# Optimization experiments

Measured on AMD Instinct MI355X. Metric: run time of the kernel, lower is better.

The kernel has to match this reference:

```python
import jax, jax.numpy as jnp
import numpy as np

N_NODES = 100000
N_EDGES = 800000
F_IN = 128
HID = 128
HEADS = 4
HEAD_DIM = HID // HEADS
LAYERS = 3
N_CLASSES = 40
NEG_SLOPE = 0.2
BN_EPS = 1e-5


def setup_inputs() -> dict:
    key = jax.random.key(0)
    ks = jax.random.split(key, 10)
    feat = jax.random.normal(ks[0], (N_NODES, F_IN), dtype=jnp.float32)
    src = jax.random.randint(ks[1], (N_EDGES,), 0, N_NODES, dtype=jnp.int32)
    dst = jax.random.randint(ks[2], (N_EDGES,), 0, N_NODES, dtype=jnp.int32)
    W_enc = jax.random.normal(ks[3], (F_IN, HID), dtype=jnp.float32) / np.sqrt(F_IN)
    b_enc = jnp.zeros((HID,), dtype=jnp.float32)
    Ws = jax.random.normal(ks[4], (LAYERS, HID, HID), dtype=jnp.float32) / np.sqrt(HID)
    attn_ls = jax.random.normal(ks[5], (LAYERS, HEADS, HEAD_DIM), dtype=jnp.float32) / np.sqrt(HEAD_DIM)
    attn_rs = jax.random.normal(ks[6], (LAYERS, HEADS, HEAD_DIM), dtype=jnp.float32) / np.sqrt(HEAD_DIM)
    biases = jnp.zeros((LAYERS, HID), dtype=jnp.float32)
    gammas = jnp.ones((LAYERS, HID), dtype=jnp.float32)
    betas = jnp.zeros((LAYERS, HID), dtype=jnp.float32)
    W_pred = jax.random.normal(ks[7], (HID, N_CLASSES), dtype=jnp.float32) / np.sqrt(HID)
    b_pred = jnp.zeros((N_CLASSES,), dtype=jnp.float32)
    return {"feat": feat, "src": src, "dst": dst, "W_enc": W_enc, "b_enc": b_enc,
            "Ws": Ws, "attn_ls": attn_ls, "attn_rs": attn_rs, "biases": biases,
            "gammas": gammas, "betas": betas, "W_pred": W_pred, "b_pred": b_pred}


def _gat_layer(h, src, dst, W, a_l, a_r, bias, n_nodes):
    # h: [N, HID] -> projected per-head features [N, H, D]
    hf = (h @ W).reshape(n_nodes, HEADS, HEAD_DIM)
    el = jnp.sum(hf * a_l, axis=-1)  # [N, H]
    er = jnp.sum(hf * a_r, axis=-1)  # [N, H]
    e = jax.nn.leaky_relu(el[src] + er[dst], NEG_SLOPE)  # [E, H]
    # edge softmax over incoming edges of each destination node
    m = jax.ops.segment_max(e, dst, num_segments=n_nodes)  # [N, H]
    ex = jnp.exp(e - m[dst])
    s = jax.ops.segment_sum(ex, dst, num_segments=n_nodes)  # [N, H]
    alpha = ex / s[dst]  # [E, H]
    msg = hf[src] * alpha[:, :, None]  # [E, H, D]
    out = jax.ops.segment_sum(msg, dst, num_segments=n_nodes)  # [N, H, D]
    return out.reshape(n_nodes, HEADS * HEAD_DIM) + bias


def _batchnorm(x, gamma, beta):
    mean = jnp.mean(x, axis=0)
    var = jnp.var(x, axis=0)
    return gamma * (x - mean) * jax.lax.rsqrt(var + BN_EPS) + beta


def reference(feat, src, dst, W_enc, b_enc, Ws, attn_ls, attn_rs, biases, gammas, betas, W_pred, b_pred):
    n_nodes = feat.shape[0]
    h = jax.nn.relu(feat @ W_enc + b_enc)
    h_last = None
    for i in range(Ws.shape[0]):
        h = _gat_layer(h, src, dst, Ws[i], attn_ls[i], attn_rs[i], biases[i], n_nodes)
        if h_last is not None:
            h = h + h_last
        h_last = h
        h = _batchnorm(h, gammas[i], betas[i])
        h = jax.nn.relu(h)
    return h @ W_pred + b_pred
```

## Files before the change

kernel.cpp:

```cpp
#include <hip/hip_runtime.h>

typedef __attribute__((ext_vector_type(8))) short short8;
typedef __attribute__((ext_vector_type(4))) float f32x4;

#define N_NODES 100000
#define N_EDGES 800000
#define NEG 0.2f
#define BN_EPS 1e-5f
#define AGG_GRID 2048

__device__ __forceinline__ ushort bf16b(float f) {
  unsigned u = __float_as_uint(f);
  return (ushort)((u + 0x7FFFu + ((u >> 16) & 1u)) >> 16);
}
__device__ __forceinline__ float bflo(unsigned u) { return __uint_as_float(u << 16); }
__device__ __forceinline__ float bfhi(unsigned u) { return __uint_as_float(u & 0xFFFF0000u); }

__global__ void k_hist(const int* __restrict__ dst, int* __restrict__ cnt, int e) {
  int i = blockIdx.x * blockDim.x + threadIdx.x;
  if (i < e) atomicAdd(&cnt[dst[i]], 1);
}

__global__ void k_scan1(const int* __restrict__ cnt, int* __restrict__ rowptr,
                        int* __restrict__ bsums, int n) {
  __shared__ int sm[256];
  int i = blockIdx.x * 256 + threadIdx.x;
  int v = (i < n) ? cnt[i] : 0;
  sm[threadIdx.x] = v;
  __syncthreads();
  for (int off = 1; off < 256; off <<= 1) {
    int t = (threadIdx.x >= off) ? sm[threadIdx.x - off] : 0;
    __syncthreads();
    sm[threadIdx.x] += t;
    __syncthreads();
  }
  if (i < n) rowptr[i + 1] = sm[threadIdx.x];
  if (threadIdx.x == 255) bsums[blockIdx.x] = sm[255];
}

__global__ void k_scan2(int* __restrict__ bsums, int nb) {
  __shared__ int sm[512];
  int v = (threadIdx.x < nb) ? bsums[threadIdx.x] : 0;
  sm[threadIdx.x] = v;
  __syncthreads();
  for (int off = 1; off < 512; off <<= 1) {
    int t = (threadIdx.x >= off) ? sm[threadIdx.x - off] : 0;
    __syncthreads();
    sm[threadIdx.x] += t;
    __syncthreads();
  }
  if (threadIdx.x < nb) bsums[threadIdx.x] = sm[threadIdx.x] - v;
}

__global__ void k_scan3(int* __restrict__ rowptr, const int* __restrict__ bsums,
                        int* __restrict__ cursor, int n) {
  int i = blockIdx.x * 256 + threadIdx.x;
  if (i < n) {
    int val = rowptr[i + 1] + bsums[blockIdx.x];
    rowptr[i + 1] = val;
    if (i + 1 < n) cursor[i + 1] = val;
  }
  if (i == 0) { rowptr[0] = 0; cursor[0] = 0; }
}

__global__ void k_scatter(const int* __restrict__ src, const int* __restrict__ dst,
                          int* __restrict__ cursor, int2* __restrict__ esort, int e) {
  int i = blockIdx.x * blockDim.x + threadIdx.x;
  if (i < e) {
    int d = dst[i];
    int pos = atomicAdd(&cursor[d], 1);
    esort[pos] = make_int2(src[i], d);
  }
}

__global__ void k_packW(const float* __restrict__ W_enc, const float* __restrict__ Ws,
                        ushort* __restrict__ Wp) {
  int s = blockIdx.x * 256 + threadIdx.x;
  int wi = s >> 11, s2 = s & 2047;
  int kt = s2 >> 9, nb8 = (s2 >> 6) & 7, l = s2 & 63;
  const float* Wsrc = (wi == 0) ? W_enc : Ws + (size_t)(wi - 1) * 16384;
  int n = nb8 * 16 + (l & 15);
  int k0 = kt * 32 + (l >> 4) * 8;
  unsigned pk[4];
#pragma unroll
  for (int j = 0; j < 4; ++j) {
    ushort lo = bf16b(Wsrc[(size_t)(k0 + 2 * j) * 128 + n]);
    ushort hi = bf16b(Wsrc[(size_t)(k0 + 2 * j + 1) * 128 + n]);
    pk[j] = (unsigned)lo | ((unsigned)hi << 16);
  }
  *(uint4*)&Wp[(size_t)s * 8] = make_uint4(pk[0], pk[1], pk[2], pk[3]);
}

template <int MODE>
__global__ __launch_bounds__(256) void k_mgemm(
    const float* __restrict__ Af, const ushort* __restrict__ Ab,
    const ushort* __restrict__ Wp, const float* __restrict__ bias,
    const float* __restrict__ stats, const float* __restrict__ al,
    const float* __restrict__ ar, float* __restrict__ el, float* __restrict__ er,
    ushort* __restrict__ Cb) {
  __shared__ __align__(16) ushort Al[32 * 128];
  int tid = threadIdx.x;
  int lane = tid & 63, w = tid >> 6;
  int wr = w & 1, wc = w >> 1;
  int l15 = lane & 15, l4 = lane >> 4;
  int rb = blockIdx.x * 32;

  const uint4* wp4 = (const uint4*)Wp;
  short8 bfr[4][4];
#pragma unroll
  for (int kt = 0; kt < 4; ++kt) {
#pragma unroll
    for (int nb = 0; nb < 4; ++nb) {
      uint4 t = wp4[(size_t)((kt * 8 + wc * 4 + nb) * 64 + lane)];
      bfr[kt][nb] = *(short8*)&t;
    }
  }

  {
    int row = tid >> 3;
    int c16 = (tid & 7) * 16;
    int kc0 = (tid & 7) * 2;
    char* base = (char*)Al + row * 256;
    if (MODE == 1) {
      const uint4* srcp = (const uint4*)(Ab + (size_t)(rb + row) * 128 + c16);
      uint4 v0 = srcp[0], v1 = srcp[1];
      *(uint4*)(base + ((kc0 ^ (row & 7)) << 4)) = v0;
      *(uint4*)(base + (((kc0 + 1) ^ (row & 7)) << 4)) = v1;
    } else if (MODE == 2) {
      const uint4* srcp = (const uint4*)(Ab + (size_t)(rb + row) * 128 + c16);
      uint4 v0 = srcp[0], v1 = srcp[1];
      unsigned pk[8];
#pragma unroll
      for (int j = 0; j < 4; ++j) {
        unsigned wv = ((const unsigned*)&v0)[j];
        float2 sc = *(const float2*)&stats[c16 + 2 * j];
        float2 sh = *(const float2*)&stats[128 + c16 + 2 * j];
        float x0 = fmaxf(bflo(wv) * sc.x + sh.x, 0.f);
        float x1 = fmaxf(bfhi(wv) * sc.y + sh.y, 0.f);
        pk[j] = (unsigned)bf16b(x0) | ((unsigned)bf16b(x1) << 16);
      }
#pragma unroll
      for (int j = 0; j < 4; ++j) {
        unsigned wv = ((const unsigned*)&v1)[j];
        float2 sc = *(const float2*)&stats[c16 + 8 + 2 * j];
        float2 sh = *(const float2*)&stats[128 + c16 + 8 + 2 * j];
        float x0 = fmaxf(bflo(wv) * sc.x + sh.x, 0.f);
        float x1 = fmaxf(bfhi(wv) * sc.y + sh.y, 0.f);
        pk[4 + j] = (unsigned)bf16b(x0) | ((unsigned)bf16b(x1) << 16);
      }
      *(uint4*)(base + ((kc0 ^ (row & 7)) << 4)) = make_uint4(pk[0], pk[1], pk[2], pk[3]);
      *(uint4*)(base + (((kc0 + 1) ^ (row & 7)) << 4)) = make_uint4(pk[4], pk[5], pk[6], pk[7]);
    } else {
      const float4* srcp = (const float4*)(Af + (size_t)(rb + row) * 128 + c16);
      float4 f[4];
#pragma unroll
      for (int j = 0; j < 4; ++j) f[j] = srcp[j];
      unsigned pk[8];
#pragma unroll
      for (int j = 0; j < 4; ++j) {
        pk[2 * j] = (unsigned)bf16b(f[j].x) | ((unsigned)bf16b(f[j].y) << 16);
        pk[2 * j + 1] = (unsigned)bf16b(f[j].z) | ((unsigned)bf16b(f[j].w) << 16);
      }
      *(uint4*)(base + ((kc0 ^ (row & 7)) << 4)) = make_uint4(pk[0], pk[1], pk[2], pk[3]);
      *(uint4*)(base + (((kc0 + 1) ^ (row & 7)) << 4)) = make_uint4(pk[4], pk[5], pk[6], pk[7]);
    }
  }
  __syncthreads();

  f32x4 acc[4];
#pragma unroll
  for (int nb = 0; nb < 4; ++nb) acc[nb] = (f32x4){0.f, 0.f, 0.f, 0.f};
  int arow = 16 * wr + l15;
  const char* abase = (const char*)Al + arow * 256;
  int sw = arow & 7;
#pragma unroll
  for (int kt = 0; kt < 4; ++kt) {
    short8 af = *(const short8*)(abase + (((kt * 4 + l4) ^ sw) << 4));
    acc[0] = __builtin_amdgcn_mfma_f32_16x16x32_bf16(af, bfr[kt][0], acc[0], 0, 0, 0);
    acc[1] = __builtin_amdgcn_mfma_f32_16x16x32_bf16(af, bfr[kt][1], acc[1], 0, 0, 0);
    acc[2] = __builtin_amdgcn_mfma_f32_16x16x32_bf16(af, bfr[kt][2], acc[2], 0, 0, 0);
    acc[3] = __builtin_amdgcn_mfma_f32_16x16x32_bf16(af, bfr[kt][3], acc[3], 0, 0, 0);
  }

  float alv0 = 0, alv1 = 0, alv2 = 0, alv3 = 0;
  float arv0 = 0, arv1 = 0, arv2 = 0, arv3 = 0;
  float bv0 = 0, bv1 = 0, bv2 = 0, bv3 = 0;
  if (MODE != 0) {
    alv0 = al[64 * wc + l15];      arv0 = ar[64 * wc + l15];
    alv1 = al[64 * wc + 16 + l15]; arv1 = ar[64 * wc + 16 + l15];
    alv2 = al[64 * wc + 32 + l15]; arv2 = ar[64 * wc + 32 + l15];
    alv3 = al[64 * wc + 48 + l15]; arv3 = ar[64 * wc + 48 + l15];
  } else {
    bv0 = bias[64 * wc + l15];      bv1 = bias[64 * wc + 16 + l15];
    bv2 = bias[64 * wc + 32 + l15]; bv3 = bias[64 * wc + 48 + l15];
  }
  int row0 = rb + 16 * wr + 4 * l4;
#pragma unroll
  for (int i = 0; i < 4; ++i) {
    int row = row0 + i;
    if (MODE != 0) {
      float pl0 = acc[0][i] * alv0 + acc[1][i] * alv1;
      float pr0 = acc[0][i] * arv0 + acc[1][i] * arv1;
      float pl1 = acc[2][i] * alv2 + acc[3][i] * alv3;
      float pr1 = acc[2][i] * arv2 + acc[3][i] * arv3;
#pragma unroll
      for (int o = 1; o < 16; o <<= 1) {
        pl0 += __shfl_xor(pl0, o); pr0 += __shfl_xor(pr0, o);
        pl1 += __shfl_xor(pl1, o); pr1 += __shfl_xor(pr1, o);
      }
      if (l15 == 0) {
        el[(size_t)row * 4 + 2 * wc] = pl0;     er[(size_t)row * 4 + 2 * wc] = pr0;
        el[(size_t)row * 4 + 2 * wc + 1] = pl1; er[(size_t)row * 4 + 2 * wc + 1] = pr1;
      }
    }
    float v0 = acc[0][i], v1 = acc[1][i], v2 = acc[2][i], v3 = acc[3][i];
    if (MODE == 0) {
      v0 = fmaxf(v0 + bv0, 0.f); v1 = fmaxf(v1 + bv1, 0.f);
      v2 = fmaxf(v2 + bv2, 0.f); v3 = fmaxf(v3 + bv3, 0.f);
    }
    size_t rbase = (size_t)row * 128 + 64 * wc + l15;
    Cb[rbase] = bf16b(v0);
    Cb[rbase + 16] = bf16b(v1);
    Cb[rbase + 32] = bf16b(v2);
    Cb[rbase + 48] = bf16b(v3);
  }
}

__global__ __launch_bounds__(256) void k_elmax1(const float* __restrict__ el,
                                                float4* __restrict__ part, int n) {
  int gid = blockIdx.x * 256 + threadIdx.x;
  float4 m = make_float4(-1e30f, -1e30f, -1e30f, -1e30f);
  for (int i = gid; i < n; i += 128 * 256) {
    float4 v = *(const float4*)&el[(size_t)4 * i];
    m.x = fmaxf(m.x, v.x); m.y = fmaxf(m.y, v.y);
    m.z = fmaxf(m.z, v.z); m.w = fmaxf(m.w, v.w);
  }
  __shared__ float4 sm[256];
  sm[threadIdx.x] = m;
  __syncthreads();
  for (int off = 128; off; off >>= 1) {
    if (threadIdx.x < off) {
      float4 o = sm[threadIdx.x + off];
      sm[threadIdx.x].x = fmaxf(sm[threadIdx.x].x, o.x);
      sm[threadIdx.x].y = fmaxf(sm[threadIdx.x].y, o.y);
      sm[threadIdx.x].z = fmaxf(sm[threadIdx.x].z, o.z);
      sm[threadIdx.x].w = fmaxf(sm[threadIdx.x].w, o.w);
    }
    __syncthreads();
  }
  if (threadIdx.x == 0) part[blockIdx.x] = sm[0];
}

__global__ void k_elmax2(const float4* __restrict__ part, float* __restrict__ elmax) {
  __shared__ float4 sm[128];
  int t = threadIdx.x;
  sm[t] = part[t];
  __syncthreads();
  for (int off = 64; off; off >>= 1) {
    if (t < off) {
      float4 o = sm[t + off];
      sm[t].x = fmaxf(sm[t].x, o.x);
      sm[t].y = fmaxf(sm[t].y, o.y);
      sm[t].z = fmaxf(sm[t].z, o.z);
      sm[t].w = fmaxf(sm[t].w, o.w);
    }
    __syncthreads();
  }
  if (t == 0) {
    elmax[0] = sm[0].x; elmax[1] = sm[0].y;
    elmax[2] = sm[0].z; elmax[3] = sm[0].w;
  }
}

__global__ __launch_bounds__(256) void k_edgew(
    const int2* __restrict__ esort, const float* __restrict__ el,
    const float* __restrict__ er, const float* __restrict__ elmax,
    float4* __restrict__ wgt, int e) {
  int j = blockIdx.x * 256 + threadIdx.x;
  if (j >= e) return;
  int2 sd = esort[j];
  float4 elv = *(const float4*)&el[(size_t)4 * sd.x];
  float4 erv = *(const float4*)&er[(size_t)4 * sd.y];
  float m0 = elmax[0] + erv.x;
  float m1 = elmax[1] + erv.y;
  float m2 = elmax[2] + erv.z;
  float m3 = elmax[3] + erv.w;
  m0 = fmaxf(m0, NEG * m0); m1 = fmaxf(m1, NEG * m1);
  m2 = fmaxf(m2, NEG * m2); m3 = fmaxf(m3, NEG * m3);
  float e0 = elv.x + erv.x; e0 = fmaxf(e0, NEG * e0);
  float e1 = elv.y + erv.y; e1 = fmaxf(e1, NEG * e1);
  float e2 = elv.z + erv.z; e2 = fmaxf(e2, NEG * e2);
  float e3 = elv.w + erv.w; e3 = fmaxf(e3, NEG * e3);
  float4 wv;
  wv.x = __expf(e0 - m0); wv.y = __expf(e1 - m1);
  wv.z = __expf(e2 - m2); wv.w = __expf(e3 - m3);
  wgt[j] = wv;
}

__global__ __launch_bounds__(256, 8) void k_aggregate(
    const ushort* __restrict__ hf, const float4* __restrict__ wgt,
    const int* __restrict__ rowptr, const int2* __restrict__ esort,
    const float* __restrict__ bias, ushort* __restrict__ hpre,
    float* __restrict__ part, int n, int addres) {
  int tid = threadIdx.x;
  int w = tid >> 6, lane = tid & 63;
  int h = lane >> 4;
  int c0 = 2 * lane;
  float2 bb = *(const float2*)&bias[c0];
  float sbn0 = 0.f, sbn1 = 0.f, qbn0 = 0.f, qbn1 = 0.f;
  for (int wid = blockIdx.x * 4 + w; wid < n; wid += AGG_GRID * 4) {
    int beg = rowptr[wid], end = rowptr[wid + 1];
    float s0 = 0.f, a00 = 0.f, a10 = 0.f;
    float s1 = 0.f, a01 = 0.f, a11 = 0.f;
    float s2 = 0.f, a02 = 0.f, a12 = 0.f;
    float s3 = 0.f, a03 = 0.f, a13 = 0.f;
    int j = beg;
    int rem = (end - beg) & 3;
    for (int t = 0; t < rem; ++t, ++j) {
      int sA = esort[j].x;
      float wA = ((const float*)(wgt + j))[h];
      unsigned hA = *(const unsigned*)(hf + (size_t)sA * 128 + c0);
      s0 += wA; a00 += wA * bflo(hA); a10 += wA * bfhi(hA);
    }
    for (; j < end; j += 4) {
      int sA = esort[j].x, sB = esort[j + 1].x, sC = esort[j + 2].x, sD = esort[j + 3].x;
      float wA = ((const float*)(wgt + j))[h];
      float wB = ((const float*)(wgt + j + 1))[h];
      float wC = ((const float*)(wgt + j + 2))[h];
      float wD = ((const float*)(wgt + j + 3))[h];
      unsigned hA = *(const unsigned*)(hf + (size_t)sA * 128 + c0);
      unsigned hB = *(const unsigned*)(hf + (size_t)sB * 128 + c0);
      unsigned hC = *(const unsigned*)(hf + (size_t)sC * 128 + c0);
      unsigned hD = *(const unsigned*)(hf + (size_t)sD * 128 + c0);
      s0 += wA; a00 += wA * bflo(hA); a10 += wA * bfhi(hA);
      s1 += wB; a01 += wB * bflo(hB); a11 += wB * bfhi(hB);
      s2 += wC; a02 += wC * bflo(hC); a12 += wC * bfhi(hC);
      s3 += wD; a03 += wD * bflo(hD); a13 += wD * bfhi(hD);
    }
    float s = (s0 + s1) + (s2 + s3);
    float inv = (end > beg) ? 1.f / s : 0.f;
    float a0 = ((a00 + a01) + (a02 + a03)) * inv;
    float a1 = ((a10 + a11) + (a12 + a13)) * inv;
    float r0 = 0.f, r1 = 0.f;
    if (addres) {
      unsigned rr = *(const unsigned*)(hpre + (size_t)wid * 128 + c0);
      r0 = bflo(rr); r1 = bfhi(rr);
    }
    float o0 = a0 + bb.x + r0, o1 = a1 + bb.y + r1;
    *(unsigned*)(hpre + (size_t)wid * 128 + c0) =
        (unsigned)bf16b(o0) | ((unsigned)bf16b(o1) << 16);
    sbn0 += o0; qbn0 += o0 * o0;
    sbn1 += o1; qbn1 += o1 * o1;
  }
  __shared__ float red_s[4][128];
  __shared__ float red_q[4][128];
  red_s[w][c0] = sbn0; red_s[w][c0 + 1] = sbn1;
  red_q[w][c0] = qbn0; red_q[w][c0 + 1] = qbn1;
  __syncthreads();
  if (tid < 128)
    part[(size_t)blockIdx.x * 256 + tid] =
        (red_s[0][tid] + red_s[1][tid]) + (red_s[2][tid] + red_s[3][tid]);
  else if (tid < 256) {
    int c = tid - 128;
    part[(size_t)blockIdx.x * 256 + tid] =
        (red_q[0][c] + red_q[1][c]) + (red_q[2][c] + red_q[3][c]);
  }
}

__global__ __launch_bounds__(320) void k_pred(
    const ushort* __restrict__ A, const float* __restrict__ stats,
    const float* __restrict__ W, const float* __restrict__ bias,
    float* __restrict__ out, int n) {
  __shared__ float Wl[128 * 40];
  __shared__ float Xl[32 * 132];
  for (int i = threadIdx.x; i < 128 * 40; i += 320) Wl[i] = W[i];
  int cg = threadIdx.x % 10;
  int rg = threadIdx.x / 10;
  float4 bv = *(const float4*)&bias[4 * cg];
  for (int rb = blockIdx.x * 32; rb < n; rb += gridDim.x * 32) {
    __syncthreads();
    for (int idx = threadIdx.x; idx < 1024; idx += 320) {
      int r = idx >> 5, c = (idx & 31) * 4;
      uint2 v = *(const uint2*)(A + (size_t)(rb + r) * 128 + c);
      float4 sc = *(const float4*)&stats[c];
      float4 sh = *(const float4*)&stats[128 + c];
      float x0 = fmaxf(bflo(v.x) * sc.x + sh.x, 0.f);
      float x1 = fmaxf(bfhi(v.x) * sc.y + sh.y, 0.f);
      float x2 = fmaxf(bflo(v.y) * sc.z + sh.z, 0.f);
      float x3 = fmaxf(bfhi(v.y) * sc.w + sh.w, 0.f);
      *(float4*)&Xl[r * 132 + c] = make_float4(x0, x1, x2, x3);
    }
    __syncthreads();
    float a0 = 0.f, a1 = 0.f, a2 = 0.f, a3 = 0.f;
#pragma unroll 4
    for (int k = 0; k < 128; ++k) {
      float x = Xl[rg * 132 + k];
      float4 w = *(float4*)&Wl[k * 40 + 4 * cg];
      a0 += x * w.x; a1 += x * w.y; a2 += x * w.z; a3 += x * w.w;
    }
    float4 o = make_float4(a0 + bv.x, a1 + bv.y, a2 + bv.z, a3 + bv.w);
    *(float4*)&out[(size_t)(rb + rg) * 40 + 4 * cg] = o;
  }
}

__global__ __launch_bounds__(256) void k_bnred(const float* __restrict__ part,
                                               float* __restrict__ colsum, int g) {
  int v = blockIdx.x;
  float acc = 0.f;
  for (int b = threadIdx.x; b < g; b += 256) acc += part[(size_t)b * 256 + v];
  __shared__ float sm[256];
  sm[threadIdx.x] = acc;
  __syncthreads();
  for (int off = 128; off; off >>= 1) {
    if (threadIdx.x < off) sm[threadIdx.x] += sm[threadIdx.x + off];
    __syncthreads();
  }
  if (threadIdx.x == 0) colsum[v] = sm[0];
}

__global__ void k_bnstat(const float* __restrict__ colsum, const float* __restrict__ gamma,
                         const float* __restrict__ beta, float* __restrict__ stats, int n) {
  int c = threadIdx.x;
  float mean = colsum[c] / n;
  float var = colsum[128 + c] / n - mean * mean;
  float rstd = rsqrtf(var + BN_EPS);
  float scale = gamma[c] * rstd;
  stats[c] = scale;
  stats[128 + c] = beta[c] - mean * scale;
}

extern "C" void kernel_launch(void* const* d_in, const int* in_sizes, int n_in,
                              void* d_out, int out_size, void* d_ws, size_t ws_size,
                              hipStream_t stream) {
  const float* feat   = (const float*)d_in[0];
  const int*   src    = (const int*)d_in[1];
  const int*   dst    = (const int*)d_in[2];
  const float* W_enc  = (const float*)d_in[3];
  const float* b_enc  = (const float*)d_in[4];
  const float* Ws     = (const float*)d_in[5];
  const float* a_ls   = (const float*)d_in[6];
  const float* a_rs   = (const float*)d_in[7];
  const float* biases = (const float*)d_in[8];
  const float* gammas = (const float*)d_in[9];
  const float* betas  = (const float*)d_in[10];
  const float* W_pred = (const float*)d_in[11];
  const float* b_pred = (const float*)d_in[12];
  float* out = (float*)d_out;

  char* p = (char*)d_ws;
  auto alloc = [&](size_t bytes) {
    char* q = p;
    p += (bytes + 255) & ~(size_t)255;
    return q;
  };
  ushort* h_bf  = (ushort*)alloc((size_t)N_NODES * 128 * 2);
  ushort* hf_bf = (ushort*)alloc((size_t)N_NODES * 128 * 2);
  ushort* hpre  = (ushort*)alloc((size_t)N_NODES * 128 * 2);
  float* el     = (float*)alloc((size_t)N_NODES * 4 * 4);
  float* er     = (float*)alloc((size_t)N_NODES * 4 * 4);
  float* part   = (float*)alloc((size_t)AGG_GRID * 256 * 4);
  float* colsum = (float*)alloc(256 * 4);
  float* stats  = (float*)alloc(256 * 4);
  ushort* Wpack = (ushort*)alloc((size_t)4 * 2048 * 16);
  float4* elpart= (float4*)alloc(128 * 16);
  float* elmax  = (float*)alloc(4 * 4);
  int* rowptr   = (int*)alloc((size_t)(N_NODES + 1) * 4);
  int* cursor   = (int*)alloc((size_t)N_NODES * 4);
  int* bsums    = (int*)alloc(512 * 4);
  int2* esort   = (int2*)alloc((size_t)N_EDGES * 8);
  float4* wgt   = (float4*)alloc((size_t)N_EDGES * 16);

  hipMemsetAsync(cursor, 0, (size_t)N_NODES * 4, stream);
  k_hist<<<(N_EDGES + 255) / 256, 256, 0, stream>>>(dst, cursor, N_EDGES);
  int nb = (N_NODES + 255) / 256;
  k_scan1<<<nb, 256, 0, stream>>>(cursor, rowptr, bsums, N_NODES);
  k_scan2<<<1, 512, 0, stream>>>(bsums, nb);
  k_scan3<<<nb, 256, 0, stream>>>(rowptr, bsums, cursor, N_NODES);
  k_scatter<<<(N_EDGES + 255) / 256, 256, 0, stream>>>(src, dst, cursor, esort, N_EDGES);

  k_packW<<<32, 256, 0, stream>>>(W_enc, Ws, Wpack);

  k_mgemm<0><<<3125, 256, 0, stream>>>(feat, nullptr, Wpack, b_enc, nullptr, nullptr,
                                       nullptr, nullptr, nullptr, h_bf);

  for (int L = 0; L < 3; ++L) {
    const float* al = a_ls + L * 128;
    const float* ar = a_rs + L * 128;
    const ushort* wp = Wpack + (size_t)(1 + L) * 16384;
    if (L == 0)
      k_mgemm<1><<<3125, 256, 0, stream>>>(nullptr, h_bf, wp, nullptr, nullptr, al, ar,
                                           el, er, hf_bf);
    else
      k_mgemm<2><<<3125, 256, 0, stream>>>(nullptr, hpre, wp, nullptr, stats, al, ar,
                                           el, er, hf_bf);
    k_elmax1<<<128, 256, 0, stream>>>(el, elpart, N_NODES);
    k_elmax2<<<1, 128, 0, stream>>>(elpart, elmax);
    k_edgew<<<(N_EDGES + 255) / 256, 256, 0, stream>>>(esort, el, er, elmax, wgt,
                                                       N_EDGES);
    k_aggregate<<<AGG_GRID, 256, 0, stream>>>(hf_bf, wgt, rowptr, esort,
                                              biases + L * 128, hpre, part, N_NODES,
                                              L > 0 ? 1 : 0);
    k_bnred<<<256, 256, 0, stream>>>(part, colsum, AGG_GRID);
    k_bnstat<<<1, 128, 0, stream>>>(colsum, gammas + L * 128, betas + L * 128, stats,
                                    N_NODES);
  }
  k_pred<<<1563, 320, 0, stream>>>(hpre, stats, W_pred, b_pred, out, N_NODES);
}
```

Before: 419.2 us.

## Fuse el-max reduction into persistent GEMM and BN stats into reduction

The projection GEMM becomes a persistent kernel with a fixed grid that loops over row tiles. It computes a per-block max of the left attention scores, which replaces the separate full pass over el. The BN column reduction and the stats computation are merged into one kernel, where the last block (found through an atomic counter) computes scale and shift. The edge scatter uses a nontemporal packed store. Together these remove launches and one memory pass per layer, at the cost of lower GEMM grid parallelism and a counter that must be reset.

```diff
diff --git a/kernel.cpp b/kernel.cpp
--- a/kernel.cpp
+++ b/kernel.cpp
@@ -8,6 +8,8 @@
 #define NEG 0.2f
 #define BN_EPS 1e-5f
 #define AGG_GRID 2048
+#define MG_GRID 1024
+#define MG_TILES 3125
 
 __device__ __forceinline__ ushort bf16b(float f) {
   unsigned u = __float_as_uint(f);
@@ -69,7 +71,9 @@
   if (i < e) {
     int d = dst[i];
     int pos = atomicAdd(&cursor[d], 1);
-    esort[pos] = make_int2(src[i], d);
+    long long packed = (long long)(((unsigned long long)(unsigned)d << 32) |
+                                   (unsigned long long)(unsigned)src[i]);
+    __builtin_nontemporal_store(packed, (long long*)&esort[pos]);
   }
 }
 
@@ -97,13 +101,12 @@
     const ushort* __restrict__ Wp, const float* __restrict__ bias,
     const float* __restrict__ stats, const float* __restrict__ al,
     const float* __restrict__ ar, float* __restrict__ el, float* __restrict__ er,
-    ushort* __restrict__ Cb) {
+    float4* __restrict__ blockmax, ushort* __restrict__ Cb) {
   __shared__ __align__(16) ushort Al[32 * 128];
   int tid = threadIdx.x;
   int lane = tid & 63, w = tid >> 6;
   int wr = w & 1, wc = w >> 1;
   int l15 = lane & 15, l4 = lane >> 4;
-  int rb = blockIdx.x * 32;
 
   const uint4* wp4 = (const uint4*)Wp;
   short8 bfr[4][4];
@@ -114,72 +117,6 @@
       uint4 t = wp4[(size_t)((kt * 8 + wc * 4 + nb) * 64 + lane)];
       bfr[kt][nb] = *(short8*)&t;
     }
-  }
-
-  {
-    int row = tid >> 3;
-    int c16 = (tid & 7) * 16;
-    int kc0 = (tid & 7) * 2;
-    char* base = (char*)Al + row * 256;
-    if (MODE == 1) {
-      const uint4* srcp = (const uint4*)(Ab + (size_t)(rb + row) * 128 + c16);
-      uint4 v0 = srcp[0], v1 = srcp[1];
-      *(uint4*)(base + ((kc0 ^ (row & 7)) << 4)) = v0;
-      *(uint4*)(base + (((kc0 + 1) ^ (row & 7)) << 4)) = v1;
-    } else if (MODE == 2) {
-      const uint4* srcp = (const uint4*)(Ab + (size_t)(rb + row) * 128 + c16);
-      uint4 v0 = srcp[0], v1 = srcp[1];
-      unsigned pk[8];
-#pragma unroll
-      for (int j = 0; j < 4; ++j) {
-        unsigned wv = ((const unsigned*)&v0)[j];
-        float2 sc = *(const float2*)&stats[c16 + 2 * j];
-        float2 sh = *(const float2*)&stats[128 + c16 + 2 * j];
-        float x0 = fmaxf(bflo(wv) * sc.x + sh.x, 0.f);
-        float x1 = fmaxf(bfhi(wv) * sc.y + sh.y, 0.f);
-        pk[j] = (unsigned)bf16b(x0) | ((unsigned)bf16b(x1) << 16);
-      }
-#pragma unroll
-      for (int j = 0; j < 4; ++j) {
-        unsigned wv = ((const unsigned*)&v1)[j];
-        float2 sc = *(const float2*)&stats[c16 + 8 + 2 * j];
-        float2 sh = *(const float2*)&stats[128 + c16 + 8 + 2 * j];
-        float x0 = fmaxf(bflo(wv) * sc.x + sh.x, 0.f);
-        float x1 = fmaxf(bfhi(wv) * sc.y + sh.y, 0.f);
-        pk[4 + j] = (unsigned)bf16b(x0) | ((unsigned)bf16b(x1) << 16);
-      }
-      *(uint4*)(base + ((kc0 ^ (row & 7)) << 4)) = make_uint4(pk[0], pk[1], pk[2], pk[3]);
-      *(uint4*)(base + (((kc0 + 1) ^ (row & 7)) << 4)) = make_uint4(pk[4], pk[5], pk[6], pk[7]);
-    } else {
-      const float4* srcp = (const float4*)(Af + (size_t)(rb + row) * 128 + c16);
-      float4 f[4];
-#pragma unroll
-      for (int j = 0; j < 4; ++j) f[j] = srcp[j];
-      unsigned pk[8];
-#pragma unroll
-      for (int j = 0; j < 4; ++j) {
-        pk[2 * j] = (unsigned)bf16b(f[j].x) | ((unsigned)bf16b(f[j].y) << 16);
-        pk[2 * j + 1] = (unsigned)bf16b(f[j].z) | ((unsigned)bf16b(f[j].w) << 16);
-      }
-      *(uint4*)(base + ((kc0 ^ (row & 7)) << 4)) = make_uint4(pk[0], pk[1], pk[2], pk[3]);
-      *(uint4*)(base + (((kc0 + 1) ^ (row & 7)) << 4)) = make_uint4(pk[4], pk[5], pk[6], pk[7]);
-    }
-  }
-  __syncthreads();
-
-  f32x4 acc[4];
-#pragma unroll
-  for (int nb = 0; nb < 4; ++nb) acc[nb] = (f32x4){0.f, 0.f, 0.f, 0.f};
-  int arow = 16 * wr + l15;
-  const char* abase = (const char*)Al + arow * 256;
-  int sw = arow & 7;
-#pragma unroll
-  for (int kt = 0; kt < 4; ++kt) {
-    short8 af = *(const short8*)(abase + (((kt * 4 + l4) ^ sw) << 4));
-    acc[0] = __builtin_amdgcn_mfma_f32_16x16x32_bf16(af, bfr[kt][0], acc[0], 0, 0, 0);
-    acc[1] = __builtin_amdgcn_mfma_f32_16x16x32_bf16(af, bfr[kt][1], acc[1], 0, 0, 0);
-    acc[2] = __builtin_amdgcn_mfma_f32_16x16x32_bf16(af, bfr[kt][2], acc[2], 0, 0, 0);
-    acc[3] = __builtin_amdgcn_mfma_f32_16x16x32_bf16(af, bfr[kt][3], acc[3], 0, 0, 0);
   }
 
   float alv0 = 0, alv1 = 0, alv2 = 0, alv3 = 0;
@@ -194,44 +131,134 @@
     bv0 = bias[64 * wc + l15];      bv1 = bias[64 * wc + 16 + l15];
     bv2 = bias[64 * wc + 32 + l15]; bv3 = bias[64 * wc + 48 + l15];
   }
-  int row0 = rb + 16 * wr + 4 * l4;
-#pragma unroll
-  for (int i = 0; i < 4; ++i) {
-    int row = row0 + i;
-    if (MODE != 0) {
-      float pl0 = acc[0][i] * alv0 + acc[1][i] * alv1;
-      float pr0 = acc[0][i] * arv0 + acc[1][i] * arv1;
-      float pl1 = acc[2][i] * alv2 + acc[3][i] * alv3;
-      float pr1 = acc[2][i] * arv2 + acc[3][i] * arv3;
-#pragma unroll
-      for (int o = 1; o < 16; o <<= 1) {
-        pl0 += __shfl_xor(pl0, o); pr0 += __shfl_xor(pr0, o);
-        pl1 += __shfl_xor(pl1, o); pr1 += __shfl_xor(pr1, o);
+
+  float gmx0 = -1e30f, gmx1 = -1e30f;
+
+  int srow = tid >> 3;
+  int c16 = (tid & 7) * 16;
+  int kc0 = (tid & 7) * 2;
+  int arow = 16 * wr + l15;
+  const char* abase = (const char*)Al + arow * 256;
+  int sw = arow & 7;
+
+  for (int tile = blockIdx.x; tile < MG_TILES; tile += MG_GRID) {
+    int rb = tile * 32;
+    __syncthreads();
+    {
+      char* base = (char*)Al + srow * 256;
+      if (MODE == 1) {
+        const uint4* srcp = (const uint4*)(Ab + (size_t)(rb + srow) * 128 + c16);
+        uint4 v0 = srcp[0], v1 = srcp[1];
+        *(uint4*)(base + ((kc0 ^ (srow & 7)) << 4)) = v0;
+        *(uint4*)(base + (((kc0 + 1) ^ (srow & 7)) << 4)) = v1;
+      } else if (MODE == 2) {
+        const uint4* srcp = (const uint4*)(Ab + (size_t)(rb + srow) * 128 + c16);
+        uint4 v0 = srcp[0], v1 = srcp[1];
+        unsigned pk[8];
+#pragma unroll
+        for (int j = 0; j < 4; ++j) {
+          unsigned wv = ((const unsigned*)&v0)[j];
+          float2 sc = *(const float2*)&stats[c16 + 2 * j];
+          float2 sh = *(const float2*)&stats[128 + c16 + 2 * j];
+          float x0 = fmaxf(bflo(wv) * sc.x + sh.x, 0.f);
+          float x1 = fmaxf(bfhi(wv) * sc.y + sh.y, 0.f);
+          pk[j] = (unsigned)bf16b(x0) | ((unsigned)bf16b(x1) << 16);
+        }
+#pragma unroll
+        for (int j = 0; j < 4; ++j) {
+          unsigned wv = ((const unsigned*)&v1)[j];
+          float2 sc = *(const float2*)&stats[c16 + 8 + 2 * j];
+          float2 sh = *(const float2*)&stats[128 + c16 + 8 + 2 * j];
+          float x0 = fmaxf(bflo(wv) * sc.x + sh.x, 0.f);
+          float x1 = fmaxf(bfhi(wv) * sc.y + sh.y, 0.f);
+          pk[4 + j] = (unsigned)bf16b(x0) | ((unsigned)bf16b(x1) << 16);
+        }
+        *(uint4*)(base + ((kc0 ^ (srow & 7)) << 4)) = make_uint4(pk[0], pk[1], pk[2], pk[3]);
+        *(uint4*)(base + (((kc0 + 1) ^ (srow & 7)) << 4)) = make_uint4(pk[4], pk[5], pk[6], pk[7]);
+      } else {
+        const float4* srcp = (const float4*)(Af + (size_t)(rb + srow) * 128 + c16);
+        float4 f[4];
+#pragma unroll
+        for (int j = 0; j < 4; ++j) f[j] = srcp[j];
+        unsigned pk[8];
+#pragma unroll
+        for (int j = 0; j < 4; ++j) {
+          pk[2 * j] = (unsigned)bf16b(f[j].x) | ((unsigned)bf16b(f[j].y) << 16);
+          pk[2 * j + 1] = (unsigned)bf16b(f[j].z) | ((unsigned)bf16b(f[j].w) << 16);
+        }
+        *(uint4*)(base + ((kc0 ^ (srow & 7)) << 4)) = make_uint4(pk[0], pk[1], pk[2], pk[3]);
+        *(uint4*)(base + (((kc0 + 1) ^ (srow & 7)) << 4)) = make_uint4(pk[4], pk[5], pk[6], pk[7]);
       }
-      if (l15 == 0) {
-        el[(size_t)row * 4 + 2 * wc] = pl0;     er[(size_t)row * 4 + 2 * wc] = pr0;
-        el[(size_t)row * 4 + 2 * wc + 1] = pl1; er[(size_t)row * 4 + 2 * wc + 1] = pr1;
+    }
+    __syncthreads();
+
+    f32x4 acc[4];
+#pragma unroll
+    for (int nb = 0; nb < 4; ++nb) acc[nb] = (f32x4){0.f, 0.f, 0.f, 0.f};
+#pragma unroll
+    for (int kt = 0; kt < 4; ++kt) {
+      short8 af = *(const short8*)(abase + (((kt * 4 + l4) ^ sw) << 4));
+      acc[0] = __builtin_amdgcn_mfma_f32_16x16x32_bf16(af, bfr[kt][0], acc[0], 0, 0, 0);
+      acc[1] = __builtin_amdgcn_mfma_f32_16x16x32_bf16(af, bfr[kt][1], acc[1], 0, 0, 0);
+      acc[2] = __builtin_amdgcn_mfma_f32_16x16x32_bf16(af, bfr[kt][2], acc[2], 0, 0, 0);
+      acc[3] = __builtin_amdgcn_mfma_f32_16x16x32_bf16(af, bfr[kt][3], acc[3], 0, 0, 0);
+    }
+
+    int row0 = rb + 16 * wr + 4 * l4;
+#pragma unroll
+    for (int i = 0; i < 4; ++i) {
+      int row = row0 + i;
+      if (MODE != 0) {
+        float pl0 = acc[0][i] * alv0 + acc[1][i] * alv1;
+        float pr0 = acc[0][i] * arv0 + acc[1][i] * arv1;
+        float pl1 = acc[2][i] * alv2 + acc[3][i] * alv3;
+        float pr1 = acc[2][i] * arv2 + acc[3][i] * arv3;
+#pragma unroll
+        for (int o = 1; o < 16; o <<= 1) {
+          pl0 += __shfl_xor(pl0, o); pr0 += __shfl_xor(pr0, o);
+          pl1 += __shfl_xor(pl1, o); pr1 += __shfl_xor(pr1, o);
+        }
+        gmx0 = fmaxf(gmx0, pl0); gmx1 = fmaxf(gmx1, pl1);
+        if (l15 == 0) {
+          el[(size_t)row * 4 + 2 * wc] = pl0;     er[(size_t)row * 4 + 2 * wc] = pr0;
+          el[(size_t)row * 4 + 2 * wc + 1] = pl1; er[(size_t)row * 4 + 2 * wc + 1] = pr1;
+        }
       }
-    }
-    float v0 = acc[0][i], v1 = acc[1][i], v2 = acc[2][i], v3 = acc[3][i];
-    if (MODE == 0) {
-      v0 = fmaxf(v0 + bv0, 0.f); v1 = fmaxf(v1 + bv1, 0.f);
-      v2 = fmaxf(v2 + bv2, 0.f); v3 = fmaxf(v3 + bv3, 0.f);
-    }
-    size_t rbase = (size_t)row * 128 + 64 * wc + l15;
-    Cb[rbase] = bf16b(v0);
-    Cb[rbase + 16] = bf16b(v1);
-    Cb[rbase + 32] = bf16b(v2);
-    Cb[rbase + 48] = bf16b(v3);
-  }
-}
-
-__global__ __launch_bounds__(256) void k_elmax1(const float* __restrict__ el,
-                                                float4* __restrict__ part, int n) {
-  int gid = blockIdx.x * 256 + threadIdx.x;
+      float v0 = acc[0][i], v1 = acc[1][i], v2 = acc[2][i], v3 = acc[3][i];
+      if (MODE == 0) {
+        v0 = fmaxf(v0 + bv0, 0.f); v1 = fmaxf(v1 + bv1, 0.f);
+        v2 = fmaxf(v2 + bv2, 0.f); v3 = fmaxf(v3 + bv3, 0.f);
+      }
+      size_t rbase = (size_t)row * 128 + 64 * wc + l15;
+      Cb[rbase] = bf16b(v0);
+      Cb[rbase + 16] = bf16b(v1);
+      Cb[rbase + 32] = bf16b(v2);
+      Cb[rbase + 48] = bf16b(v3);
+    }
+  }
+
+  if (MODE != 0) {
+    gmx0 = fmaxf(gmx0, __shfl_xor(gmx0, 16)); gmx0 = fmaxf(gmx0, __shfl_xor(gmx0, 32));
+    gmx1 = fmaxf(gmx1, __shfl_xor(gmx1, 16)); gmx1 = fmaxf(gmx1, __shfl_xor(gmx1, 32));
+    __shared__ float lm[4][2];
+    if (lane == 0) { lm[w][0] = gmx0; lm[w][1] = gmx1; }
+    __syncthreads();
+    if (tid == 0) {
+      float4 bm;
+      bm.x = fmaxf(lm[0][0], lm[1][0]);
+      bm.y = fmaxf(lm[0][1], lm[1][1]);
+      bm.z = fmaxf(lm[2][0], lm[3][0]);
+      bm.w = fmaxf(lm[2][1], lm[3][1]);
+      blockmax[blockIdx.x] = bm;
+    }
+  }
+}
+
+__global__ __launch_bounds__(256) void k_elmax2(const float4* __restrict__ bm,
+                                                float* __restrict__ elmax, int g) {
   float4 m = make_float4(-1e30f, -1e30f, -1e30f, -1e30f);
-  for (int i = gid; i < n; i += 128 * 256) {
-    float4 v = *(const float4*)&el[(size_t)4 * i];
+  for (int i = threadIdx.x; i < g; i += 256) {
+    float4 v = bm[i];
     m.x = fmaxf(m.x, v.x); m.y = fmaxf(m.y, v.y);
     m.z = fmaxf(m.z, v.z); m.w = fmaxf(m.w, v.w);
   }
@@ -248,25 +275,7 @@
     }
     __syncthreads();
   }
-  if (threadIdx.x == 0) part[blockIdx.x] = sm[0];
-}
-
-__global__ void k_elmax2(const float4* __restrict__ part, float* __restrict__ elmax) {
-  __shared__ float4 sm[128];
-  int t = threadIdx.x;
-  sm[t] = part[t];
-  __syncthreads();
-  for (int off = 64; off; off >>= 1) {
-    if (t < off) {
-      float4 o = sm[t + off];
-      sm[t].x = fmaxf(sm[t].x, o.x);
-      sm[t].y = fmaxf(sm[t].y, o.y);
-      sm[t].z = fmaxf(sm[t].z, o.z);
-      sm[t].w = fmaxf(sm[t].w, o.w);
-    }
-    __syncthreads();
-  }
-  if (t == 0) {
+  if (threadIdx.x == 0) {
     elmax[0] = sm[0].x; elmax[1] = sm[0].y;
     elmax[2] = sm[0].z; elmax[3] = sm[0].w;
   }
@@ -403,8 +412,10 @@
   }
 }
 
-__global__ __launch_bounds__(256) void k_bnred(const float* __restrict__ part,
-                                               float* __restrict__ colsum, int g) {
+__global__ __launch_bounds__(256) void k_bnred(
+    const float* __restrict__ part, float* __restrict__ colsum,
+    const float* __restrict__ gamma, const float* __restrict__ beta,
+    float* __restrict__ stats, unsigned* __restrict__ ctr, int g, int n) {
   int v = blockIdx.x;
   float acc = 0.f;
   for (int b = threadIdx.x; b < g; b += 256) acc += part[(size_t)b * 256 + v];
@@ -415,18 +426,26 @@
     if (threadIdx.x < off) sm[threadIdx.x] += sm[threadIdx.x + off];
     __syncthreads();
   }
-  if (threadIdx.x == 0) colsum[v] = sm[0];
-}
-
-__global__ void k_bnstat(const float* __restrict__ colsum, const float* __restrict__ gamma,
-                         const float* __restrict__ beta, float* __restrict__ stats, int n) {
-  int c = threadIdx.x;
-  float mean = colsum[c] / n;
-  float var = colsum[128 + c] / n - mean * mean;
-  float rstd = rsqrtf(var + BN_EPS);
-  float scale = gamma[c] * rstd;
-  stats[c] = scale;
-  stats[128 + c] = beta[c] - mean * scale;
+  __shared__ int last;
+  if (threadIdx.x == 0) {
+    colsum[v] = sm[0];
+    __threadfence();
+    last = (atomicAdd(ctr, 1u) == (unsigned)(gridDim.x - 1));
+  }
+  __syncthreads();
+  if (last) {
+    __threadfence();
+    if (threadIdx.x == 0) *ctr = 0;
+    if (threadIdx.x < 128) {
+      int c = threadIdx.x;
+      float mean = colsum[c] / n;
+      float var = colsum[128 + c] / n - mean * mean;
+      float rstd = rsqrtf(var + BN_EPS);
+      float scale = gamma[c] * rstd;
+      stats[c] = scale;
+      stats[128 + c] = beta[c] - mean * scale;
+    }
+  }
 }
 
 extern "C" void kernel_launch(void* const* d_in, const int* in_sizes, int n_in,
@@ -462,8 +481,9 @@
   float* colsum = (float*)alloc(256 * 4);
   float* stats  = (float*)alloc(256 * 4);
   ushort* Wpack = (ushort*)alloc((size_t)4 * 2048 * 16);
-  float4* elpart= (float4*)alloc(128 * 16);
+  float4* bmax  = (float4*)alloc((size_t)MG_GRID * 16);
   float* elmax  = (float*)alloc(4 * 4);
+  unsigned* ctr = (unsigned*)alloc(256);
   int* rowptr   = (int*)alloc((size_t)(N_NODES + 1) * 4);
   int* cursor   = (int*)alloc((size_t)N_NODES * 4);
   int* bsums    = (int*)alloc(512 * 4);
@@ -471,6 +491,7 @@
   float4* wgt   = (float4*)alloc((size_t)N_EDGES * 16);
 
   hipMemsetAsync(cursor, 0, (size_t)N_NODES * 4, stream);
+  hipMemsetAsync(ctr, 0, 4, stream);
   k_hist<<<(N_EDGES + 255) / 256, 256, 0, stream>>>(dst, cursor, N_EDGES);
   int nb = (N_NODES + 255) / 256;
   k_scan1<<<nb, 256, 0, stream>>>(cursor, rowptr, bsums, N_NODES);
@@ -480,29 +501,27 @@
 
   k_packW<<<32, 256, 0, stream>>>(W_enc, Ws, Wpack);
 
-  k_mgemm<0><<<3125, 256, 0, stream>>>(feat, nullptr, Wpack, b_enc, nullptr, nullptr,
-                                       nullptr, nullptr, nullptr, h_bf);
+  k_mgemm<0><<<MG_GRID, 256, 0, stream>>>(feat, nullptr, Wpack, b_enc, nullptr, nullptr,
+                                          nullptr, nullptr, nullptr, nullptr, h_bf);
 
   for (int L = 0; L < 3; ++L) {
     const float* al = a_ls + L * 128;
     const float* ar = a_rs + L * 128;
     const ushort* wp = Wpack + (size_t)(1 + L) * 16384;
     if (L == 0)
-      k_mgemm<1><<<3125, 256, 0, stream>>>(nullptr, h_bf, wp, nullptr, nullptr, al, ar,
-                                           el, er, hf_bf);
+      k_mgemm<1><<<MG_GRID, 256, 0, stream>>>(nullptr, h_bf, wp, nullptr, nullptr, al,
+                                              ar, el, er, bmax, hf_bf);
     else
-      k_mgemm<2><<<3125, 256, 0, stream>>>(nullptr, hpre, wp, nullptr, stats, al, ar,
-                                           el, er, hf_bf);
-    k_elmax1<<<128, 256, 0, stream>>>(el, elpart, N_NODES);
-    k_elmax2<<<1, 128, 0, stream>>>(elpart, elmax);
+      k_mgemm<2><<<MG_GRID, 256, 0, stream>>>(nullptr, hpre, wp, nullptr, stats, al,
+                                              ar, el, er, bmax, hf_bf);
+    k_elmax2<<<1, 256, 0, stream>>>(bmax, elmax, MG_GRID);
     k_edgew<<<(N_EDGES + 255) / 256, 256, 0, stream>>>(esort, el, er, elmax, wgt,
                                                        N_EDGES);
     k_aggregate<<<AGG_GRID, 256, 0, stream>>>(hf_bf, wgt, rowptr, esort,
                                               biases + L * 128, hpre, part, N_NODES,
                                               L > 0 ? 1 : 0);
-    k_bnred<<<256, 256, 0, stream>>>(part, colsum, AGG_GRID);
-    k_bnstat<<<1, 128, 0, stream>>>(colsum, gammas + L * 128, betas + L * 128, stats,
-                                    N_NODES);
+    k_bnred<<<256, 256, 0, stream>>>(part, colsum, gammas + L * 128, betas + L * 128,
+                                     stats, ctr, AGG_GRID, N_NODES);
   }
   k_pred<<<1563, 320, 0, stream>>>(hpre, stats, W_pred, b_pred, out, N_NODES);
 }
```

Measured after the change: 439.9 us. 4.9% more time.
